# Optimization experiments

Measured on AMD Instinct MI355X. Metric: run time of the kernel, lower is better.

Reference implementation:

```python
import jax, jax.numpy as jnp
import numpy as np

B = 512          # batch_size
C = 4            # num_classes
N = 16384        # grid unknowns per sample (128x128)
H = 0.0078125    # grid spacing h = 1/128


def setup_inputs() -> dict:
    key = jax.random.key(0)
    k1, k2, k3 = jax.random.split(key, 3)
    coefficients = jax.random.uniform(k1, (B, N), dtype=jnp.float32)  # positive -> A SPD
    predictions = jax.random.normal(k2, (B, C, N), dtype=jnp.float32)
    targets = jax.random.normal(k3, (B, N, C), dtype=jnp.float32)
    return {"coefficients": coefficients, "predictions": predictions, "targets": targets}


def reference(coefficients, predictions, targets):
    # A = diag(h^2 * coefficients[i]); exploit diagonality: A @ v == a * v.
    a = (H * H) * coefficients                      # [B, N] diagonal of A per sample
    preds = predictions.reshape(B, C, -1)           # predictions.view(batch_size, num_classes, -1)

    # Modified Gram-Schmidt in the A-inner product, vectorized over batch.
    ortho = []
    for j in range(C):                              # tiny fixed loop over classes
        v = preds[:, j, :]                          # [B, N]
        for e in ortho:
            proj = jnp.sum(v * (a * e), axis=-1, keepdims=True)  # <v, A e>
            v = v - proj * e
        n2 = jnp.sum(v * a * v, axis=-1, keepdims=True)          # <v, A v>
        safe = jnp.where(n2 > 0, n2, jnp.float32(1.0))
        v = jnp.where(n2 > 0, v * jax.lax.rsqrt(safe), v)        # normalize iff <v,Av> > 0
        ortho.append(v)
    Cm = jnp.stack(ortho, axis=1)                   # [B, C, N]

    # M = C_i @ A @ targets[i] for each sample -> [B, C, C]
    M = jnp.einsum('bcn,bnm->bcm', Cm * a[:, None, :], targets)
    per_sample = (jnp.float32(4.0) - jnp.sum(M * M, axis=(1, 2))) / jnp.float32(4.0)
    return jnp.mean(per_sample)
```

## Files before the change

kernel.cpp:

```cpp
#include <hip/hip_runtime.h>

#define BSZ 512
#define NC  4
#define NN  16384
#define H2  (0.0078125f * 0.0078125f)

#define BLK 512

__device__ __forceinline__ void accum_elem(float a,
                                           float p0, float p1, float p2, float p3,
                                           float tx, float ty, float tz, float tw,
                                           float* acc)
{
    float ap0 = a * p0, ap1 = a * p1, ap2 = a * p2, ap3 = a * p3;
    acc[0]  += ap0 * p0;  acc[1]  += ap0 * p1;  acc[2]  += ap0 * p2;  acc[3]  += ap0 * p3;
    acc[4]  += ap1 * p1;  acc[5]  += ap1 * p2;  acc[6]  += ap1 * p3;
    acc[7]  += ap2 * p2;  acc[8]  += ap2 * p3;
    acc[9]  += ap3 * p3;
    acc[10] += ap0 * tx;  acc[11] += ap0 * ty;  acc[12] += ap0 * tz;  acc[13] += ap0 * tw;
    acc[14] += ap1 * tx;  acc[15] += ap1 * ty;  acc[16] += ap1 * tz;  acc[17] += ap1 * tw;
    acc[18] += ap2 * tx;  acc[19] += ap2 * ty;  acc[20] += ap2 * tz;  acc[21] += ap2 * tw;
    acc[22] += ap3 * tx;  acc[23] += ap3 * ty;  acc[24] += ap3 * tz;  acc[25] += ap3 * tw;
}

__global__ __launch_bounds__(BLK)
void loss_main(const float* __restrict__ coef,
               const float* __restrict__ pred,
               const float* __restrict__ targ,
               float* __restrict__ per_sample)
{
    const int b   = blockIdx.x;
    const int tid = threadIdx.x;

    const float4* __restrict__ c4 = (const float4*)(coef + (size_t)b * NN);
    const float4* __restrict__ q0 = (const float4*)(pred + (size_t)b * NC * NN + 0 * NN);
    const float4* __restrict__ q1 = (const float4*)(pred + (size_t)b * NC * NN + 1 * NN);
    const float4* __restrict__ q2 = (const float4*)(pred + (size_t)b * NC * NN + 2 * NN);
    const float4* __restrict__ q3 = (const float4*)(pred + (size_t)b * NC * NN + 3 * NN);
    const float4* __restrict__ t4 = (const float4*)(targ + (size_t)b * NN * NC);

    float acc[26];
#pragma unroll
    for (int k = 0; k < 26; ++k) acc[k] = 0.f;

    for (int i = tid; i < NN / 4; i += BLK) {
        float4 cc = c4[i];
        float4 a0 = q0[i];
        float4 a1 = q1[i];
        float4 a2 = q2[i];
        float4 a3 = q3[i];
        float4 t0 = t4[4 * i + 0];
        float4 t1 = t4[4 * i + 1];
        float4 t2 = t4[4 * i + 2];
        float4 t3 = t4[4 * i + 3];

        accum_elem(H2 * cc.x, a0.x, a1.x, a2.x, a3.x, t0.x, t0.y, t0.z, t0.w, acc);
        accum_elem(H2 * cc.y, a0.y, a1.y, a2.y, a3.y, t1.x, t1.y, t1.z, t1.w, acc);
        accum_elem(H2 * cc.z, a0.z, a1.z, a2.z, a3.z, t2.x, t2.y, t2.z, t2.w, acc);
        accum_elem(H2 * cc.w, a0.w, a1.w, a2.w, a3.w, t3.x, t3.y, t3.z, t3.w, acc);
    }

    const int lane = tid & 63;
    const int wv   = tid >> 6;
    __shared__ float red[26][8];

#pragma unroll
    for (int k = 0; k < 26; ++k) {
        float v = acc[k];
#pragma unroll
        for (int o = 32; o > 0; o >>= 1) v += __shfl_down(v, o, 64);
        if (lane == 0) red[k][wv] = v;
    }
    __syncthreads();

    if (tid == 0) {
        float s[26];
#pragma unroll
        for (int k = 0; k < 26; ++k) {
            float v = 0.f;
#pragma unroll
            for (int w = 0; w < 8; ++w) v += red[k][w];
            s[k] = v;
        }

        float Gm[4][4];
        Gm[0][0] = s[0];
        Gm[0][1] = Gm[1][0] = s[1];
        Gm[0][2] = Gm[2][0] = s[2];
        Gm[0][3] = Gm[3][0] = s[3];
        Gm[1][1] = s[4];
        Gm[1][2] = Gm[2][1] = s[5];
        Gm[1][3] = Gm[3][1] = s[6];
        Gm[2][2] = s[7];
        Gm[2][3] = Gm[3][2] = s[8];
        Gm[3][3] = s[9];

        float Tm[4][4];
#pragma unroll
        for (int i = 0; i < 4; ++i)
#pragma unroll
            for (int m = 0; m < 4; ++m) Tm[i][m] = s[10 + 4 * i + m];

        float u[4][4];
#pragma unroll
        for (int j = 0; j < 4; ++j) {
            float w[4];
#pragma unroll
            for (int i = 0; i < 4; ++i) w[i] = (i == j) ? 1.f : 0.f;
#pragma unroll
            for (int k = 0; k < 4; ++k) {
                if (k < j) {
                    float proj = 0.f;
#pragma unroll
                    for (int i = 0; i < 4; ++i) {
                        float gu = 0.f;
#pragma unroll
                        for (int l = 0; l < 4; ++l) gu += Gm[i][l] * u[k][l];
                        proj += w[i] * gu;
                    }
#pragma unroll
                    for (int i = 0; i < 4; ++i) w[i] -= proj * u[k][i];
                }
            }
            float n2 = 0.f;
#pragma unroll
            for (int i = 0; i < 4; ++i) {
                float gw = 0.f;
#pragma unroll
                for (int l = 0; l < 4; ++l) gw += Gm[i][l] * w[l];
                n2 += w[i] * gw;
            }
            float sc = (n2 > 0.f) ? rsqrtf(n2) : 1.f;
#pragma unroll
            for (int i = 0; i < 4; ++i) u[j][i] = w[i] * sc;
        }

        float ssum = 0.f;
#pragma unroll
        for (int c = 0; c < 4; ++c) {
#pragma unroll
            for (int m = 0; m < 4; ++m) {
                float M = 0.f;
#pragma unroll
                for (int i = 0; i < 4; ++i) M += u[c][i] * Tm[i][m];
                ssum += M * M;
            }
        }
        per_sample[b] = (4.f - ssum) * 0.25f;
    }
}

__global__ __launch_bounds__(BSZ)
void reduce_final(const float* __restrict__ ps, float* __restrict__ out)
{
    const int tid = threadIdx.x;
    float v = ps[tid];
#pragma unroll
    for (int o = 32; o > 0; o >>= 1) v += __shfl_down(v, o, 64);
    __shared__ float red[8];
    if ((tid & 63) == 0) red[tid >> 6] = v;
    __syncthreads();
    if (tid == 0) {
        float ssum = 0.f;
#pragma unroll
        for (int w = 0; w < 8; ++w) ssum += red[w];
        out[0] = ssum / (float)BSZ;
    }
}

extern "C" void kernel_launch(void* const* d_in, const int* in_sizes, int n_in,
                              void* d_out, int out_size, void* d_ws, size_t ws_size,
                              hipStream_t stream)
{
    const float* coef = (const float*)d_in[0];
    const float* pred = (const float*)d_in[1];
    const float* targ = (const float*)d_in[2];
    float* out = (float*)d_out;
    float* ps  = (float*)d_ws;

    loss_main<<<BSZ, BLK, 0, stream>>>(coef, pred, targ, ps);
    reduce_final<<<1, BSZ, 0, stream>>>(ps, out);
}
```

Measured before the change: 303.2 us.

## Split each sample across two blocks and move Gram-Schmidt into final kernel

Each sample's reduction is now spread over two blocks (1024 blocks total), each writing 26 partial sums. A single final kernel combines the partials and runs the small 4x4 Gram-Schmidt per sample, one thread per sample, before the mean reduction. The loop becomes fully unrolled with a fixed trip count, and launch bounds ask for more resident blocks. The aim is better CU occupancy and more memory-level parallelism on a bandwidth-bound stream, at the cost of extra partial writes and a more serial final kernel.

```diff
diff --git a/kernel.cpp b/kernel.cpp
--- a/kernel.cpp
+++ b/kernel.cpp
@@ -5,7 +5,10 @@
 #define NN  16384
 #define H2  (0.0078125f * 0.0078125f)
 
-#define BLK 512
+#define BLK   512
+#define SPLIT 2
+#define GROUPS_PER_BLOCK (NN / 4 / SPLIT)
+#define ITERS (GROUPS_PER_BLOCK / BLK)
 
 __device__ __forceinline__ void accum_elem(float a,
                                            float p0, float p1, float p2, float p3,
@@ -23,13 +26,15 @@
     acc[22] += ap3 * tx;  acc[23] += ap3 * ty;  acc[24] += ap3 * tz;  acc[25] += ap3 * tw;
 }
 
-__global__ __launch_bounds__(BLK)
-void loss_main(const float* __restrict__ coef,
+__global__ __launch_bounds__(BLK, 8)
+void loss_part(const float* __restrict__ coef,
                const float* __restrict__ pred,
                const float* __restrict__ targ,
-               float* __restrict__ per_sample)
-{
-    const int b   = blockIdx.x;
+               float* __restrict__ partial)
+{
+    const int blk = blockIdx.x;
+    const int b   = blk / SPLIT;
+    const int s   = blk % SPLIT;
     const int tid = threadIdx.x;
 
     const float4* __restrict__ c4 = (const float4*)(coef + (size_t)b * NN);
@@ -39,11 +44,15 @@
     const float4* __restrict__ q3 = (const float4*)(pred + (size_t)b * NC * NN + 3 * NN);
     const float4* __restrict__ t4 = (const float4*)(targ + (size_t)b * NN * NC);
 
+    const int g0 = s * GROUPS_PER_BLOCK;
+
     float acc[26];
 #pragma unroll
     for (int k = 0; k < 26; ++k) acc[k] = 0.f;
 
-    for (int i = tid; i < NN / 4; i += BLK) {
+#pragma unroll
+    for (int k = 0; k < ITERS; ++k) {
+        const int i = g0 + k * BLK + tid;
         float4 cc = c4[i];
         float4 a0 = q0[i];
         float4 a1 = q1[i];
@@ -73,98 +82,106 @@
     }
     __syncthreads();
 
-    if (tid == 0) {
-        float s[26];
-#pragma unroll
-        for (int k = 0; k < 26; ++k) {
-            float v = 0.f;
-#pragma unroll
-            for (int w = 0; w < 8; ++w) v += red[k][w];
-            s[k] = v;
-        }
-
-        float Gm[4][4];
-        Gm[0][0] = s[0];
-        Gm[0][1] = Gm[1][0] = s[1];
-        Gm[0][2] = Gm[2][0] = s[2];
-        Gm[0][3] = Gm[3][0] = s[3];
-        Gm[1][1] = s[4];
-        Gm[1][2] = Gm[2][1] = s[5];
-        Gm[1][3] = Gm[3][1] = s[6];
-        Gm[2][2] = s[7];
-        Gm[2][3] = Gm[3][2] = s[8];
-        Gm[3][3] = s[9];
-
-        float Tm[4][4];
-#pragma unroll
-        for (int i = 0; i < 4; ++i)
-#pragma unroll
-            for (int m = 0; m < 4; ++m) Tm[i][m] = s[10 + 4 * i + m];
-
-        float u[4][4];
-#pragma unroll
-        for (int j = 0; j < 4; ++j) {
-            float w[4];
-#pragma unroll
-            for (int i = 0; i < 4; ++i) w[i] = (i == j) ? 1.f : 0.f;
-#pragma unroll
-            for (int k = 0; k < 4; ++k) {
-                if (k < j) {
-                    float proj = 0.f;
-#pragma unroll
-                    for (int i = 0; i < 4; ++i) {
-                        float gu = 0.f;
-#pragma unroll
-                        for (int l = 0; l < 4; ++l) gu += Gm[i][l] * u[k][l];
-                        proj += w[i] * gu;
-                    }
-#pragma unroll
-                    for (int i = 0; i < 4; ++i) w[i] -= proj * u[k][i];
+    if (tid < 26) {
+        float v = 0.f;
+#pragma unroll
+        for (int w = 0; w < 8; ++w) v += red[tid][w];
+        partial[(size_t)blk * 26 + tid] = v;
+    }
+}
+
+__global__ __launch_bounds__(BSZ)
+void loss_final(const float* __restrict__ partial, float* __restrict__ out)
+{
+    const int b = threadIdx.x;
+
+    float s[26];
+#pragma unroll
+    for (int k = 0; k < 26; ++k) {
+        float v = 0.f;
+#pragma unroll
+        for (int p = 0; p < SPLIT; ++p)
+            v += partial[(size_t)(b * SPLIT + p) * 26 + k];
+        s[k] = v;
+    }
+
+    float Gm[4][4];
+    Gm[0][0] = s[0];
+    Gm[0][1] = Gm[1][0] = s[1];
+    Gm[0][2] = Gm[2][0] = s[2];
+    Gm[0][3] = Gm[3][0] = s[3];
+    Gm[1][1] = s[4];
+    Gm[1][2] = Gm[2][1] = s[5];
+    Gm[1][3] = Gm[3][1] = s[6];
+    Gm[2][2] = s[7];
+    Gm[2][3] = Gm[3][2] = s[8];
+    Gm[3][3] = s[9];
+
+    float Tm[4][4];
+#pragma unroll
+    for (int i = 0; i < 4; ++i)
+#pragma unroll
+        for (int m = 0; m < 4; ++m) Tm[i][m] = s[10 + 4 * i + m];
+
+    float u[4][4];
+#pragma unroll
+    for (int j = 0; j < 4; ++j) {
+        float w[4];
+#pragma unroll
+        for (int i = 0; i < 4; ++i) w[i] = (i == j) ? 1.f : 0.f;
+#pragma unroll
+        for (int k = 0; k < 4; ++k) {
+            if (k < j) {
+                float proj = 0.f;
+#pragma unroll
+                for (int i = 0; i < 4; ++i) {
+                    float gu = 0.f;
+#pragma unroll
+                    for (int l = 0; l < 4; ++l) gu += Gm[i][l] * u[k][l];
+                    proj += w[i] * gu;
                 }
-            }
-            float n2 = 0.f;
-#pragma unroll
-            for (int i = 0; i < 4; ++i) {
-                float gw = 0.f;
-#pragma unroll
-                for (int l = 0; l < 4; ++l) gw += Gm[i][l] * w[l];
-                n2 += w[i] * gw;
-            }
-            float sc = (n2 > 0.f) ? rsqrtf(n2) : 1.f;
-#pragma unroll
-            for (int i = 0; i < 4; ++i) u[j][i] = w[i] * sc;
-        }
-
-        float ssum = 0.f;
-#pragma unroll
-        for (int c = 0; c < 4; ++c) {
-#pragma unroll
-            for (int m = 0; m < 4; ++m) {
-                float M = 0.f;
-#pragma unroll
-                for (int i = 0; i < 4; ++i) M += u[c][i] * Tm[i][m];
-                ssum += M * M;
+#pragma unroll
+                for (int i = 0; i < 4; ++i) w[i] -= proj * u[k][i];
             }
         }
-        per_sample[b] = (4.f - ssum) * 0.25f;
-    }
-}
-
-__global__ __launch_bounds__(BSZ)
-void reduce_final(const float* __restrict__ ps, float* __restrict__ out)
-{
-    const int tid = threadIdx.x;
-    float v = ps[tid];
-#pragma unroll
-    for (int o = 32; o > 0; o >>= 1) v += __shfl_down(v, o, 64);
+        float n2 = 0.f;
+#pragma unroll
+        for (int i = 0; i < 4; ++i) {
+            float gw = 0.f;
+#pragma unroll
+            for (int l = 0; l < 4; ++l) gw += Gm[i][l] * w[l];
+            n2 += w[i] * gw;
+        }
+        float sc = (n2 > 0.f) ? rsqrtf(n2) : 1.f;
+#pragma unroll
+        for (int i = 0; i < 4; ++i) u[j][i] = w[i] * sc;
+    }
+
+    float ssum = 0.f;
+#pragma unroll
+    for (int c = 0; c < 4; ++c) {
+#pragma unroll
+        for (int m = 0; m < 4; ++m) {
+            float M = 0.f;
+#pragma unroll
+            for (int i = 0; i < 4; ++i) M += u[c][i] * Tm[i][m];
+            ssum += M * M;
+        }
+    }
+    float ps = (4.f - ssum) * 0.25f;
+
+    const int lane = b & 63;
+    const int wv   = b >> 6;
+#pragma unroll
+    for (int o = 32; o > 0; o >>= 1) ps += __shfl_down(ps, o, 64);
     __shared__ float red[8];
-    if ((tid & 63) == 0) red[tid >> 6] = v;
+    if (lane == 0) red[wv] = ps;
     __syncthreads();
-    if (tid == 0) {
-        float ssum = 0.f;
-#pragma unroll
-        for (int w = 0; w < 8; ++w) ssum += red[w];
-        out[0] = ssum / (float)BSZ;
+    if (b == 0) {
+        float tot = 0.f;
+#pragma unroll
+        for (int w = 0; w < 8; ++w) tot += red[w];
+        out[0] = tot / (float)BSZ;
     }
 }
 
@@ -176,8 +193,8 @@
     const float* pred = (const float*)d_in[1];
     const float* targ = (const float*)d_in[2];
     float* out = (float*)d_out;
-    float* ps  = (float*)d_ws;
-
-    loss_main<<<BSZ, BLK, 0, stream>>>(coef, pred, targ, ps);
-    reduce_final<<<1, BSZ, 0, stream>>>(ps, out);
-}
+    float* partial = (float*)d_ws;
+
+    loss_part<<<BSZ * SPLIT, BLK, 0, stream>>>(coef, pred, targ, partial);
+    loss_final<<<1, BSZ, 0, stream>>>(partial, out);
+}
```

Measured after the change: 611.4 us. 102% more time.
